# Kernel tuning notes

Measured on AMD Instinct MI355X. Metric: run time of the kernel, lower is better.

The kernel has to match this reference:

```python
import jax, jax.numpy as jnp
import numpy as np

EPS = 1e-12  # matches torch F.normalize default eps


def _l2_normalize(x, axis=-1):
    norm = jnp.sqrt(jnp.sum(x * x, axis=axis, keepdims=True))
    return x / jnp.maximum(norm, EPS)


def setup_inputs() -> dict:
    key = jax.random.key(0)
    k1, k2 = jax.random.split(key)
    B, D, P = 8192, 512, 32768
    z_context = jax.random.normal(k1, (B, D), dtype=jnp.float32)
    prototypes = jax.random.normal(k2, (P, D), dtype=jnp.float32) * 0.02
    return {"z_context": z_context, "prototypes": prototypes, "topk": 3}


def reference(z_context, prototypes, topk):
    # Cosine similarity: normalize queries and prototype bank, then GEMM.
    z_norm = _l2_normalize(z_context, axis=-1)          # [B, D]
    p_norm = _l2_normalize(prototypes, axis=-1)         # [P, D]
    sim = jnp.einsum('bd,pd->bp', z_norm, p_norm)       # [B, P]
    k = min(topk, prototypes.shape[0])
    topk_val, topk_idx = jax.lax.top_k(sim, k)          # [B, k] each
    return sim, topk_idx, topk_val
```

## Files before the change

kernel.cpp:

```cpp
#include <hip/hip_runtime.h>
#include <float.h>
#include <stdint.h>

#define D_DIM 512

typedef __attribute__((ext_vector_type(8))) short bf16x8;
typedef __attribute__((ext_vector_type(4))) float f32x4;

#define GLD_LDS16(g, l)                                              \
    __builtin_amdgcn_global_load_lds(                                \
        (const __attribute__((address_space(1))) void*)(g),          \
        (__attribute__((address_space(3))) void*)(l), 16, 0, 0)

__device__ __forceinline__ uint32_t pk_bf16(float a, float b) {
    uint32_t ua = __builtin_bit_cast(uint32_t, a) + 0x8000u;
    uint32_t ub = __builtin_bit_cast(uint32_t, b) + 0x8000u;
    return (ua >> 16) | (ub & 0xFFFF0000u);
}

#define INS4(val, idx, tv, ti)                                        \
    if ((val) > tv[3]) {                                              \
        int p_ = 3;                                                   \
        if ((val) > tv[2]) { tv[3] = tv[2]; ti[3] = ti[2]; p_ = 2; }  \
        if ((val) > tv[1]) { tv[2] = tv[1]; ti[2] = ti[1]; p_ = 1; }  \
        if ((val) > tv[0]) { tv[1] = tv[0]; ti[1] = ti[0]; p_ = 0; }  \
        tv[p_] = (val); ti[p_] = (idx);                               \
    }

__global__ __launch_bounds__(256) void convert_norm_kernel(
        const float* __restrict__ X, unsigned short* __restrict__ Xb,
        float* __restrict__ r, int R) {
    int row = blockIdx.x * 4 + (threadIdx.x >> 6);
    if (row >= R) return;
    int lane = threadIdx.x & 63;
    const float* x = X + (size_t)row * D_DIM + lane * 8;
    float4 f0 = *(const float4*)(x);
    float4 f1 = *(const float4*)(x + 4);
    float s = f0.x*f0.x + f0.y*f0.y + f0.z*f0.z + f0.w*f0.w
            + f1.x*f1.x + f1.y*f1.y + f1.z*f1.z + f1.w*f1.w;
#pragma unroll
    for (int off = 32; off; off >>= 1) s += __shfl_xor(s, off);
    float rv = 1.0f / fmaxf(sqrtf(s), 1e-12f);
    if (lane == 0) r[row] = rv;
    uint4 w;
    w.x = pk_bf16(f0.x * rv, f0.y * rv);
    w.y = pk_bf16(f0.z * rv, f0.w * rv);
    w.z = pk_bf16(f1.x * rv, f1.y * rv);
    w.w = pk_bf16(f1.z * rv, f1.w * rv);
    *(uint4*)(Xb + (size_t)row * D_DIM + lane * 8) = w;
}

__global__ __launch_bounds__(512, 2) void gemm256_fused(
        const unsigned short* __restrict__ Zb,
        const unsigned short* __restrict__ Pb,
        float* __restrict__ sim, uint2* __restrict__ part, int Pn) {
    extern __shared__ __align__(16) unsigned char SH[];
    uint4* S = (uint4*)SH;

    int bi = blockIdx.x;
    int mb, nb;
    if (gridDim.x == 4096) {
        int xcd = bi & 7, r = bi >> 3;
        mb = xcd * 4 + (r & 3);
        nb = r >> 2;
    } else {
        int nt = Pn >> 8;
        nb = bi % nt; mb = bi / nt;
    }
    const int bm = mb << 8, bn = nb << 8;

    const int tid = threadIdx.x;
    const int lane = tid & 63;
    const int wid = tid >> 6;
    const int wr = wid >> 2;
    const int wc = wid & 3;
    const int ln15 = lane & 15, hi = lane >> 4;

    const int fl0 = tid, fl1 = 512 + tid;
    const int rl0 = fl0 >> 3, rl1 = fl1 >> 3;
    const int cg0 = (fl0 & 7) ^ (rl0 & 7);
    const int cg1 = (fl1 & 7) ^ (rl1 & 7);

    const unsigned short* pA0q0 = Zb + (size_t)(bm + rl0) * D_DIM + cg0 * 8;
    const unsigned short* pA0q1 = Zb + (size_t)(bm + rl1) * D_DIM + cg1 * 8;
    const unsigned short* pA1q0 = Zb + (size_t)(bm + 128 + rl0) * D_DIM + cg0 * 8;
    const unsigned short* pA1q1 = Zb + (size_t)(bm + 128 + rl1) * D_DIM + cg1 * 8;
    const unsigned short* pB0q0 = Pb + (size_t)(bn + rl0) * D_DIM + cg0 * 8;
    const unsigned short* pB0q1 = Pb + (size_t)(bn + rl1) * D_DIM + cg1 * 8;
    const unsigned short* pB1q0 = Pb + (size_t)(bn + 128 + rl0) * D_DIM + cg0 * 8;
    const unsigned short* pB1q1 = Pb + (size_t)(bn + 128 + rl1) * D_DIM + cg1 * 8;

    const int dA0q0 = fl0,        dA0q1 = fl1;
    const int dA1q0 = 1024 + fl0, dA1q1 = 1024 + fl1;
    const int dB0q0 = 4096 + fl0, dB0q1 = 4096 + fl1;
    const int dB1q0 = 5120 + fl0, dB1q1 = 5120 + fl1;

    const int sw0 = hi ^ (ln15 & 7);
    const int sw1 = (4 + hi) ^ (ln15 & 7);
    int aOff[8], bOff[4];
#pragma unroll
    for (int m = 0; m < 8; ++m) aOff[m] = (wr * 128 + m * 16 + ln15) * 8;
#pragma unroll
    for (int n = 0; n < 4; ++n) bOff[n] = 4096 + (wc * 64 + n * 16 + ln15) * 8;

    f32x4 acc[8][4] = {};

    GLD_LDS16(pA0q0, &S[dA0q0]); GLD_LDS16(pA0q1, &S[dA0q1]);
    GLD_LDS16(pA1q0, &S[dA1q0]); GLD_LDS16(pA1q1, &S[dA1q1]);
    GLD_LDS16(pB0q0, &S[dB0q0]); GLD_LDS16(pB0q1, &S[dB0q1]);
    GLD_LDS16(pB1q0, &S[dB1q0]); GLD_LDS16(pB1q1, &S[dB1q1]);
    pA0q0 += 64; pA0q1 += 64; pA1q0 += 64; pA1q1 += 64;
    pB0q0 += 64; pB0q1 += 64; pB1q0 += 64; pB1q1 += 64;
    asm volatile("s_waitcnt vmcnt(0)" ::: "memory");
    __builtin_amdgcn_s_barrier();

#pragma unroll 1
    for (int t = 0; t < 8; ++t) {
        const int db = (t & 1) * 2048;
        const int dn = ((t + 1) & 1) * 2048;
        const bool more = (t < 7);
#pragma unroll
        for (int p = 0; p < 4; ++p) {
            const int mh = p >> 1, nh = p & 1;
            bf16x8 av[4][2], bv[2][2];
#pragma unroll
            for (int mi = 0; mi < 4; ++mi) {
                av[mi][0] = __builtin_bit_cast(bf16x8, S[db + aOff[mh * 4 + mi] + sw0]);
                av[mi][1] = __builtin_bit_cast(bf16x8, S[db + aOff[mh * 4 + mi] + sw1]);
            }
#pragma unroll
            for (int ni = 0; ni < 2; ++ni) {
                bv[ni][0] = __builtin_bit_cast(bf16x8, S[db + bOff[nh * 2 + ni] + sw0]);
                bv[ni][1] = __builtin_bit_cast(bf16x8, S[db + bOff[nh * 2 + ni] + sw1]);
            }
            if (p == 0 && more) {
                GLD_LDS16(pB0q0, &S[dn + dB0q0]); GLD_LDS16(pB0q1, &S[dn + dB0q1]);
                GLD_LDS16(pA0q0, &S[dn + dA0q0]); GLD_LDS16(pA0q1, &S[dn + dA0q1]);
                pB0q0 += 64; pB0q1 += 64; pA0q0 += 64; pA0q1 += 64;
            }
            if (p == 1 && more) {
                GLD_LDS16(pB1q0, &S[dn + dB1q0]); GLD_LDS16(pB1q1, &S[dn + dB1q1]);
                GLD_LDS16(pA1q0, &S[dn + dA1q0]); GLD_LDS16(pA1q1, &S[dn + dA1q1]);
                pB1q0 += 64; pB1q1 += 64; pA1q0 += 64; pA1q1 += 64;
            }
            __builtin_amdgcn_s_barrier();
            asm volatile("s_waitcnt lgkmcnt(0)" ::: "memory");
            __builtin_amdgcn_sched_barrier(0);
            __builtin_amdgcn_s_setprio(1);
#pragma unroll
            for (int kk = 0; kk < 2; ++kk)
#pragma unroll
                for (int mi = 0; mi < 4; ++mi)
#pragma unroll
                    for (int ni = 0; ni < 2; ++ni)
                        acc[mh * 4 + mi][nh * 2 + ni] =
                            __builtin_amdgcn_mfma_f32_16x16x32_bf16(
                                av[mi][kk], bv[ni][kk],
                                acc[mh * 4 + mi][nh * 2 + ni], 0, 0, 0);
            __builtin_amdgcn_s_setprio(0);
            __builtin_amdgcn_sched_barrier(0);
            if (p < 3) __builtin_amdgcn_s_barrier();
        }
        if (more) asm volatile("s_waitcnt vmcnt(0)" ::: "memory");
        __builtin_amdgcn_s_barrier();
    }

    float* T = (float*)SH;
    const int NB = Pn >> 8;
    const int r = tid >> 2;
    const int g = tid & 3;
#pragma unroll 1
    for (int hf = 0; hf < 2; ++hf) {
        float tv[4]; int ti[4];
#pragma unroll
        for (int k = 0; k < 4; ++k) { tv[k] = -FLT_MAX; ti[k] = 0x7FFFFFFF; }
#pragma unroll 1
        for (int ch = 0; ch < 2; ++ch) {
            __syncthreads();
            if (wr == hf && (wc >> 1) == ch) {
#pragma unroll
                for (int m = 0; m < 8; ++m)
#pragma unroll
                    for (int n = 0; n < 4; ++n)
                        *(f32x4*)&T[((wc & 1) * 64 + n * 16 + ln15) * 132
                                    + m * 16 + hi * 4] = acc[m][n];
            }
            __syncthreads();
            const int colBase = bn + ch * 128;
            float* srow = sim + (size_t)(bm + hf * 128 + r) * Pn + colBase;
#pragma unroll
            for (int j = 0; j < 8; ++j) {
                const int c0 = j * 16 + g * 4;
                float e0 = T[(c0 + 0) * 132 + r];
                float e1 = T[(c0 + 1) * 132 + r];
                float e2 = T[(c0 + 2) * 132 + r];
                float e3 = T[(c0 + 3) * 132 + r];
                float4 o; o.x = e0; o.y = e1; o.z = e2; o.w = e3;
                *(float4*)&srow[c0] = o;
                float mg = fmaxf(fmaxf(e0, e1), fmaxf(e2, e3));
                if (mg > tv[3]) {
                    INS4(e0, colBase + c0 + 0, tv, ti);
                    INS4(e1, colBase + c0 + 1, tv, ti);
                    INS4(e2, colBase + c0 + 2, tv, ti);
                    INS4(e3, colBase + c0 + 3, tv, ti);
                }
            }
        }
#pragma unroll
        for (int st = 1; st <= 2; st <<= 1) {
            float ov0 = __shfl_xor(tv[0], st), ov1 = __shfl_xor(tv[1], st);
            float ov2 = __shfl_xor(tv[2], st), ov3 = __shfl_xor(tv[3], st);
            int oi0 = __shfl_xor(ti[0], st), oi1 = __shfl_xor(ti[1], st);
            int oi2 = __shfl_xor(ti[2], st), oi3 = __shfl_xor(ti[3], st);
            INS4(ov0, oi0, tv, ti);
            INS4(ov1, oi1, tv, ti);
            INS4(ov2, oi2, tv, ti);
            INS4(ov3, oi3, tv, ti);
        }
        if (g == 0) {
            size_t o = ((size_t)(bm + hf * 128 + r) * NB + nb) * 4;
#pragma unroll
            for (int k = 0; k < 4; ++k)
                part[o + k] =
                    make_uint2(__builtin_bit_cast(uint32_t, tv[k]), (uint32_t)ti[k]);
        }
    }
}

__global__ __launch_bounds__(256) void topk_reduce(const uint2* __restrict__ part,
        const float* __restrict__ Z, const float* __restrict__ Pm,
        const float* __restrict__ rz, const float* __restrict__ rp,
        float* __restrict__ oidx, float* __restrict__ oval, int Pn, int NB) {
    int row = blockIdx.x * 4 + (threadIdx.x >> 6);
    int lane = threadIdx.x & 63;
    const uint2* pr = part + (size_t)row * NB * 4;

    float v[8]; int ix[8];
#pragma unroll
    for (int j = 0; j < 8; ++j) { v[j] = -FLT_MAX; ix[j] = -1; }

    const int total = NB * 4;
    for (int c = lane; c < total; c += 64) {
        uint2 u = pr[c];
        float val = __builtin_bit_cast(float, u.x);
        if (val > v[7]) {
            int idx = (int)u.y;
            int pos = 7;
#pragma unroll
            for (int j = 6; j >= 0; --j) {
                if (val > v[j]) { v[j+1] = v[j]; ix[j+1] = ix[j]; pos = j; }
            }
            v[pos] = val; ix[pos] = idx;
        }
    }

    int cand[8];
#pragma unroll
    for (int k = 0; k < 8; ++k) {
        float bv = v[0]; int bi2 = ix[0];
#pragma unroll
        for (int off = 32; off; off >>= 1) {
            float ov = __shfl_xor(bv, off);
            int oi = __shfl_xor(bi2, off);
            if (ov > bv || (ov == bv && oi >= 0 && (unsigned)oi < (unsigned)bi2)) {
                bv = ov; bi2 = oi;
            }
        }
        cand[k] = bi2;
        if (bi2 == ix[0]) {
#pragma unroll
            for (int j = 0; j < 7; ++j) { v[j] = v[j+1]; ix[j] = ix[j+1]; }
            v[7] = -FLT_MAX; ix[7] = -1;
        }
    }

    float zv[8];
    const float* zrow = Z + (size_t)row * D_DIM + lane * 8;
#pragma unroll
    for (int j = 0; j < 8; ++j) zv[j] = zrow[j];
    float rzv = rz[row];

    float ex[8];
#pragma unroll
    for (int c = 0; c < 8; ++c) {
        int idx = cand[c];
        const float* prow = Pm + (size_t)idx * D_DIM + lane * 8;
        float s = 0.f;
#pragma unroll
        for (int j = 0; j < 8; ++j) s += zv[j] * prow[j];
#pragma unroll
        for (int off = 32; off; off >>= 1) s += __shfl_xor(s, off);
        ex[c] = s * rzv * rp[idx];
    }

    bool used[8] = {};
#pragma unroll
    for (int k = 0; k < 3; ++k) {
        float bv = -FLT_MAX; int bi2 = Pn; int bc = 0;
#pragma unroll
        for (int c = 0; c < 8; ++c) {
            if (!used[c] && (ex[c] > bv || (ex[c] == bv && cand[c] < bi2))) {
                bv = ex[c]; bi2 = cand[c]; bc = c;
            }
        }
        used[bc] = true;
        if (lane == 0) {
            oidx[(size_t)row * 3 + k] = (float)bi2;
            oval[(size_t)row * 3 + k] = bv;
        }
    }
}

template <bool FUSE>
__global__ __launch_bounds__(256, 4) void gemm_lds_bf16(
        const unsigned short* __restrict__ Zb,
        const unsigned short* __restrict__ Pb,
        float* __restrict__ sim, uint2* __restrict__ part, int Pn) {
    __shared__ __align__(16) unsigned char SHs[32768];
    uint4* S = (uint4*)SHs;

    int bi = blockIdx.x;
    int mb, nb;
    if (gridDim.x == 16384) {
        int xcd = bi & 7;
        int r = bi >> 3;
        mb = xcd * 8 + (r & 7);
        nb = r >> 3;
    } else {
        nb = bi % (Pn / 128);
        mb = bi / (Pn / 128);
    }
    const int bm = mb * 128, bn = nb * 128;

    const int tid = threadIdx.x;
    const int lane = tid & 63;
    const int wid = tid >> 6;
    const int wr = wid >> 1, wc = wid & 1;
    const int ln15 = lane & 15, hi = lane >> 4;

    const unsigned short* gA[2];
    const unsigned short* gB[2];
    int ldsIdx[2];
#pragma unroll
    for (int q = 0; q < 2; ++q) {
        int flat = q * 256 + tid;
        int row = flat >> 2;
        int c = flat & 3;
        int cg = c ^ (row & 3);
        gA[q] = Zb + (size_t)(bm + row) * D_DIM + cg * 8;
        gB[q] = Pb + (size_t)(bn + row) * D_DIM + cg * 8;
        ldsIdx[q] = flat;
    }

    f32x4 acc[4][4] = {};

#pragma unroll
    for (int q = 0; q < 2; ++q) {
        GLD_LDS16(gA[q], &S[ldsIdx[q]]);
        GLD_LDS16(gB[q], &S[512 + ldsIdx[q]]);
        gA[q] += 32;
        gB[q] += 32;
    }

    int cur = 0;
#pragma unroll 1
    for (int s8 = 0; s8 < 16; ++s8) {
        const int nxt = cur ^ 1;
        if (s8 < 15) {
#pragma unroll
            for (int q = 0; q < 2; ++q) {
                GLD_LDS16(gA[q], &S[nxt * 1024 + ldsIdx[q]]);
                GLD_LDS16(gB[q], &S[nxt * 1024 + 512 + ldsIdx[q]]);
                gA[q] += 32;
                gB[q] += 32;
            }
            asm volatile("s_waitcnt vmcnt(4)" ::: "memory");
        } else {
            asm volatile("s_waitcnt vmcnt(0)" ::: "memory");
        }
        __builtin_amdgcn_s_barrier();
        __builtin_amdgcn_sched_barrier(0);

        const int sb = cur * 1024;
        __builtin_amdgcn_s_setprio(1);
        bf16x8 av[4], bv[4];
#pragma unroll
        for (int t = 0; t < 4; ++t) {
            int arow = wr * 64 + t * 16 + ln15;
            av[t] = __builtin_bit_cast(bf16x8,
                    S[sb + arow * 4 + (hi ^ (arow & 3))]);
            int brow = wc * 64 + t * 16 + ln15;
            bv[t] = __builtin_bit_cast(bf16x8,
                    S[sb + 512 + brow * 4 + (hi ^ (brow & 3))]);
        }
#pragma unroll
        for (int i = 0; i < 4; ++i)
#pragma unroll
            for (int j = 0; j < 4; ++j)
                acc[i][j] = __builtin_amdgcn_mfma_f32_16x16x32_bf16(
                    av[i], bv[j], acc[i][j], 0, 0, 0);
        __builtin_amdgcn_s_setprio(0);
        __builtin_amdgcn_sched_barrier(0);
        __builtin_amdgcn_s_barrier();
        cur = nxt;
    }

#pragma unroll
    for (int i = 0; i < 4; ++i) {
#pragma unroll
        for (int rr = 0; rr < 4; ++rr) {
            int row = bm + wr * 64 + i * 16 + hi * 4 + rr;
#pragma unroll
            for (int j = 0; j < 4; ++j) {
                int col = bn + wc * 64 + j * 16 + ln15;
                sim[(size_t)row * Pn + col] = acc[i][j][rr];
            }
        }
    }

    if constexpr (FUSE) {
        float* T = (float*)SHs;
        uint2* M = (uint2*)(SHs + 17408);
        const int NB = Pn >> 7;
        const int r = tid & 63;
        const int q = tid >> 6;
#pragma unroll 1
        for (int hf = 0; hf < 2; ++hf) {
            float rv[4]; int ri[4];
#pragma unroll
            for (int k = 0; k < 4; ++k) { rv[k] = -FLT_MAX; ri[k] = 0x7FFFFFFF; }
#pragma unroll 1
            for (int ch = 0; ch < 2; ++ch) {
                __syncthreads();
                if (wr == hf && wc == ch) {
#pragma unroll
                    for (int i = 0; i < 4; ++i)
#pragma unroll
                        for (int j = 0; j < 4; ++j)
                            *(f32x4*)&T[(j * 16 + ln15) * 68 + i * 16 + hi * 4]
                                = acc[i][j];
                }
                __syncthreads();
                float tv[4]; int ti[4];
#pragma unroll
                for (int k = 0; k < 4; ++k) { tv[k] = -FLT_MAX; ti[k] = 0x7FFFFFFF; }
#pragma unroll
                for (int c4 = 0; c4 < 16; c4 += 4) {
                    float e0 = T[(q * 16 + c4 + 0) * 68 + r];
                    float e1 = T[(q * 16 + c4 + 1) * 68 + r];
                    float e2 = T[(q * 16 + c4 + 2) * 68 + r];
                    float e3 = T[(q * 16 + c4 + 3) * 68 + r];
                    float mg = fmaxf(fmaxf(e0, e1), fmaxf(e2, e3));
                    if (mg > tv[3]) {
                        int cb = bn + ch * 64 + q * 16 + c4;
                        INS4(e0, cb + 0, tv, ti);
                        INS4(e1, cb + 1, tv, ti);
                        INS4(e2, cb + 2, tv, ti);
                        INS4(e3, cb + 3, tv, ti);
                    }
                }
#pragma unroll
                for (int k = 0; k < 4; ++k)
                    M[q * 256 + k * 64 + r] =
                        make_uint2(__builtin_bit_cast(uint32_t, tv[k]), (uint32_t)ti[k]);
                __syncthreads();
                if (tid < 64) {
#pragma unroll
                    for (int qq = 0; qq < 4; ++qq)
#pragma unroll
                        for (int k = 0; k < 4; ++k) {
                            uint2 u = M[qq * 256 + k * 64 + tid];
                            float val = __builtin_bit_cast(float, u.x);
                            INS4(val, (int)u.y, rv, ri);
                        }
                }
            }
            if (tid < 64) {
                size_t o = ((size_t)(bm + hf * 64 + tid) * NB + nb) * 4;
#pragma unroll
                for (int k = 0; k < 4; ++k)
                    part[o + k] =
                        make_uint2(__builtin_bit_cast(uint32_t, rv[k]), (uint32_t)ri[k]);
            }
        }
    }
}

__global__ __launch_bounds__(256) void rnorm_kernel(const float* __restrict__ X,
                                                    float* __restrict__ r, int R) {
    int row = blockIdx.x * 4 + (threadIdx.x >> 6);
    if (row >= R) return;
    int lane = threadIdx.x & 63;
    const float* x = X + (size_t)row * D_DIM;
    float s = 0.f;
#pragma unroll
    for (int t = 0; t < 2; ++t) {
        float4 v = *(const float4*)(x + (t * 64 + lane) * 4);
        s += v.x * v.x + v.y * v.y + v.z * v.z + v.w * v.w;
    }
#pragma unroll
    for (int off = 32; off; off >>= 1) s += __shfl_xor(s, off);
    if (lane == 0) r[row] = 1.0f / fmaxf(sqrtf(s), 1e-12f);
}

__global__ __launch_bounds__(256, 2) void gemm_bf16_sim(const float* __restrict__ Z,
        const float* __restrict__ Pm, const float* __restrict__ rz,
        const float* __restrict__ rp, float* __restrict__ sim, int Pn) {
    __shared__ uint4 As16[1024];
    __shared__ uint4 Bs16[1024];
    int bi = blockIdx.x;
    int nb = bi % (Pn / 128);
    int mb = bi / (Pn / 128);
    const int bm = mb * 128, bn = nb * 128;
    const int tid = threadIdx.x;
    const int srow = tid >> 1;
    const int half = tid & 1;
    const float* aP = Z  + (size_t)(bm + srow) * D_DIM + half * 32;
    const float* bP = Pm + (size_t)(bn + srow) * D_DIM + half * 32;
    const int lane = tid & 63;
    const int wid = tid >> 6;
    const int wr = wid >> 1, wc = wid & 1;
    const int ln15 = lane & 15, hi = lane >> 4;
    f32x4 acc[4][4] = {};
    float4 f[8], g[8];
#pragma unroll
    for (int q = 0; q < 8; ++q) {
        f[q] = *(const float4*)(aP + q * 4);
        g[q] = *(const float4*)(bP + q * 4);
    }
#pragma unroll 1
    for (int s = 0; s < 8; ++s) {
#pragma unroll
        for (int q8 = 0; q8 < 4; ++q8) {
            uint4 wa, wb;
            wa.x = pk_bf16(f[2*q8].x,   f[2*q8].y);
            wa.y = pk_bf16(f[2*q8].z,   f[2*q8].w);
            wa.z = pk_bf16(f[2*q8+1].x, f[2*q8+1].y);
            wa.w = pk_bf16(f[2*q8+1].z, f[2*q8+1].w);
            wb.x = pk_bf16(g[2*q8].x,   g[2*q8].y);
            wb.y = pk_bf16(g[2*q8].z,   g[2*q8].w);
            wb.z = pk_bf16(g[2*q8+1].x, g[2*q8+1].y);
            wb.w = pk_bf16(g[2*q8+1].z, g[2*q8+1].w);
            int colByte = half * 64 + q8 * 16;
            int idx = srow * 8 + ((colByte ^ ((srow & 7) << 4)) >> 4);
            As16[idx] = wa;
            Bs16[idx] = wb;
        }
        __syncthreads();
        if (s < 7) {
            int k0 = (s + 1) * 64;
#pragma unroll
            for (int q = 0; q < 8; ++q) {
                f[q] = *(const float4*)(aP + k0 + q * 4);
                g[q] = *(const float4*)(bP + k0 + q * 4);
            }
        }
#pragma unroll
        for (int kk = 0; kk < 2; ++kk) {
            bf16x8 av[4], bv[4];
            const int cb = kk * 64 + hi * 16;
#pragma unroll
            for (int t = 0; t < 4; ++t) {
                int arow = wr * 64 + t * 16 + ln15;
                av[t] = __builtin_bit_cast(bf16x8,
                        As16[arow * 8 + ((cb ^ ((arow & 7) << 4)) >> 4)]);
                int brow = wc * 64 + t * 16 + ln15;
                bv[t] = __builtin_bit_cast(bf16x8,
                        Bs16[brow * 8 + ((cb ^ ((brow & 7) << 4)) >> 4)]);
            }
#pragma unroll
            for (int i = 0; i < 4; ++i)
#pragma unroll
                for (int j = 0; j < 4; ++j)
                    acc[i][j] = __builtin_amdgcn_mfma_f32_16x16x32_bf16(
                        av[i], bv[j], acc[i][j], 0, 0, 0);
        }
        __syncthreads();
    }
    float rpv[4];
#pragma unroll
    for (int j = 0; j < 4; ++j) rpv[j] = rp[bn + wc * 64 + j * 16 + ln15];
#pragma unroll
    for (int i = 0; i < 4; ++i) {
#pragma unroll
        for (int rr = 0; rr < 4; ++rr) {
            int row = bm + wr * 64 + i * 16 + hi * 4 + rr;
            float rzv = rz[row];
#pragma unroll
            for (int j = 0; j < 4; ++j) {
                int col = bn + wc * 64 + j * 16 + ln15;
                sim[(size_t)row * Pn + col] = acc[i][j][rr] * rzv * rpv[j];
            }
        }
    }
}

__global__ __launch_bounds__(256) void topk_refine(const float* __restrict__ sim,
        const float* __restrict__ Z, const float* __restrict__ Pm,
        const float* __restrict__ rz, const float* __restrict__ rp,
        float* __restrict__ oidx, float* __restrict__ oval, int Pn) {
    int row = blockIdx.x * 4 + (threadIdx.x >> 6);
    int lane = threadIdx.x & 63;
    const float* rptr = sim + (size_t)row * Pn;

    float v[8]; int ix[8];
#pragma unroll
    for (int j = 0; j < 8; ++j) { v[j] = -FLT_MAX; ix[j] = -1; }

    const int iters = Pn >> 8;
    for (int t = 0; t < iters; ++t) {
        int base = t * 256 + lane * 4;
        float4 q = *(const float4*)(rptr + base);
        float vals[4] = {q.x, q.y, q.z, q.w};
#pragma unroll
        for (int e = 0; e < 4; ++e) {
            float val = vals[e];
            if (val > v[7]) {
                int idx = base + e;
                int pos = 7;
#pragma unroll
                for (int j = 6; j >= 0; --j) {
                    if (val > v[j]) { v[j+1] = v[j]; ix[j+1] = ix[j]; pos = j; }
                }
                v[pos] = val; ix[pos] = idx;
            }
        }
    }

    int cand[8];
#pragma unroll
    for (int k = 0; k < 8; ++k) {
        float bv = v[0]; int bi2 = ix[0];
#pragma unroll
        for (int off = 32; off; off >>= 1) {
            float ov = __shfl_xor(bv, off);
            int oi = __shfl_xor(bi2, off);
            if (ov > bv || (ov == bv && oi >= 0 && (unsigned)oi < (unsigned)bi2)) {
                bv = ov; bi2 = oi;
            }
        }
        cand[k] = bi2;
        if (bi2 == ix[0]) {
#pragma unroll
            for (int j = 0; j < 7; ++j) { v[j] = v[j+1]; ix[j] = ix[j+1]; }
            v[7] = -FLT_MAX; ix[7] = -1;
        }
    }

    float zv[8];
    const float* zrow = Z + (size_t)row * D_DIM + lane * 8;
#pragma unroll
    for (int j = 0; j < 8; ++j) zv[j] = zrow[j];
    float rzv = rz[row];

    float ex[8];
#pragma unroll
    for (int c = 0; c < 8; ++c) {
        int idx = cand[c];
        const float* prow = Pm + (size_t)idx * D_DIM + lane * 8;
        float s = 0.f;
#pragma unroll
        for (int j = 0; j < 8; ++j) s += zv[j] * prow[j];
#pragma unroll
        for (int off = 32; off; off >>= 1) s += __shfl_xor(s, off);
        ex[c] = s * rzv * rp[idx];
    }

    bool used[8] = {};
#pragma unroll
    for (int k = 0; k < 3; ++k) {
        float bv = -FLT_MAX; int bi2 = Pn; int bc = 0;
#pragma unroll
        for (int c = 0; c < 8; ++c) {
            if (!used[c] && (ex[c] > bv || (ex[c] == bv && cand[c] < bi2))) {
                bv = ex[c]; bi2 = cand[c]; bc = c;
            }
        }
        used[bc] = true;
        if (lane == 0) {
            oidx[(size_t)row * 3 + k] = (float)bi2;
            oval[(size_t)row * 3 + k] = bv;
        }
    }
}

extern "C" void kernel_launch(void* const* d_in, const int* in_sizes, int n_in,
                              void* d_out, int out_size, void* d_ws, size_t ws_size,
                              hipStream_t stream) {
    const float* Z  = (const float*)d_in[0];
    const float* Pm = (const float*)d_in[1];
    const int B  = in_sizes[0] / D_DIM;
    const int Pn = in_sizes[1] / D_DIM;

    float* sim  = (float*)d_out;
    float* oidx = sim + (size_t)B * Pn;
    float* oval = oidx + (size_t)B * 3;

    float* rz = (float*)d_ws;
    float* rp = rz + B;
    unsigned short* Zb = (unsigned short*)(rp + Pn);
    unsigned short* Pb = Zb + (size_t)B * D_DIM;
    uint2* part = (uint2*)(Pb + (size_t)Pn * D_DIM);

    const size_t need_bf16 = (size_t)(B + Pn) * 4 + (size_t)(B + Pn) * D_DIM * 2;
    const size_t need256 = need_bf16 + (size_t)B * (Pn >> 8) * 4 * sizeof(uint2);
    const size_t need128 = need_bf16 + (size_t)B * (Pn >> 7) * 4 * sizeof(uint2);

    bool big = false;
    if ((B & 255) == 0 && (Pn & 255) == 0 && ws_size >= need256) {
        big = (hipFuncSetAttribute((const void*)gemm256_fused,
                   hipFuncAttributeMaxDynamicSharedMemorySize,
                   131072) == hipSuccess);
    }

    if (big) {
        convert_norm_kernel<<<B / 4, 256, 0, stream>>>(Z, Zb, rz, B);
        convert_norm_kernel<<<Pn / 4, 256, 0, stream>>>(Pm, Pb, rp, Pn);
        gemm256_fused<<<(B / 256) * (Pn / 256), 512, 131072, stream>>>(
            Zb, Pb, sim, part, Pn);
        topk_reduce<<<B / 4, 256, 0, stream>>>(part, Z, Pm, rz, rp,
                                               oidx, oval, Pn, Pn >> 8);
    } else if (ws_size >= need128) {
        convert_norm_kernel<<<B / 4, 256, 0, stream>>>(Z, Zb, rz, B);
        convert_norm_kernel<<<Pn / 4, 256, 0, stream>>>(Pm, Pb, rp, Pn);
        gemm_lds_bf16<true><<<(B / 128) * (Pn / 128), 256, 0, stream>>>(
            Zb, Pb, sim, part, Pn);
        topk_reduce<<<B / 4, 256, 0, stream>>>(part, Z, Pm, rz, rp,
                                               oidx, oval, Pn, Pn >> 7);
    } else if (ws_size >= need_bf16) {
        convert_norm_kernel<<<B / 4, 256, 0, stream>>>(Z, Zb, rz, B);
        convert_norm_kernel<<<Pn / 4, 256, 0, stream>>>(Pm, Pb, rp, Pn);
        gemm_lds_bf16<false><<<(B / 128) * (Pn / 128), 256, 0, stream>>>(
            Zb, Pb, sim, nullptr, Pn);
        topk_refine<<<B / 4, 256, 0, stream>>>(sim, Z, Pm, rz, rp, oidx, oval, Pn);
    } else {
        rnorm_kernel<<<B / 4, 256, 0, stream>>>(Z, rz, B);
        rnorm_kernel<<<Pn / 4, 256, 0, stream>>>(Pm, rp, Pn);
        gemm_bf16_sim<<<(B / 128) * (Pn / 128), 256, 0, stream>>>(
            Z, Pm, rz, rp, sim, Pn);
        topk_refine<<<B / 4, 256, 0, stream>>>(sim, Z, Pm, rz, rp, oidx, oval, Pn);
    }
}
```

Before: 699.3 us.

## Use four-stage K=32 LDS pipeline and nontemporal stores for sim output

The main loop moves from a two-buffer K=64 pipeline to a four-buffer ring of K=32 stages. Three stages of global-to-LDS loads are kept in flight, with vmcnt waits matched to the number of outstanding loads. The per-stage sub-phase split and the extra barriers inside each stage are removed, and the swizzle changes to a 4-group XOR. The sim matrix writes now use nontemporal stores to avoid polluting the cache. Each stage does less MFMA work per barrier, so synchronisation overhead per unit of compute may go up.

```diff
diff --git a/kernel.cpp b/kernel.cpp
--- a/kernel.cpp
+++ b/kernel.cpp
@@ -76,94 +76,71 @@
     const int wc = wid & 3;
     const int ln15 = lane & 15, hi = lane >> 4;
 
-    const int fl0 = tid, fl1 = 512 + tid;
-    const int rl0 = fl0 >> 3, rl1 = fl1 >> 3;
-    const int cg0 = (fl0 & 7) ^ (rl0 & 7);
-    const int cg1 = (fl1 & 7) ^ (rl1 & 7);
-
-    const unsigned short* pA0q0 = Zb + (size_t)(bm + rl0) * D_DIM + cg0 * 8;
-    const unsigned short* pA0q1 = Zb + (size_t)(bm + rl1) * D_DIM + cg1 * 8;
-    const unsigned short* pA1q0 = Zb + (size_t)(bm + 128 + rl0) * D_DIM + cg0 * 8;
-    const unsigned short* pA1q1 = Zb + (size_t)(bm + 128 + rl1) * D_DIM + cg1 * 8;
-    const unsigned short* pB0q0 = Pb + (size_t)(bn + rl0) * D_DIM + cg0 * 8;
-    const unsigned short* pB0q1 = Pb + (size_t)(bn + rl1) * D_DIM + cg1 * 8;
-    const unsigned short* pB1q0 = Pb + (size_t)(bn + 128 + rl0) * D_DIM + cg0 * 8;
-    const unsigned short* pB1q1 = Pb + (size_t)(bn + 128 + rl1) * D_DIM + cg1 * 8;
-
-    const int dA0q0 = fl0,        dA0q1 = fl1;
-    const int dA1q0 = 1024 + fl0, dA1q1 = 1024 + fl1;
-    const int dB0q0 = 4096 + fl0, dB0q1 = 4096 + fl1;
-    const int dB1q0 = 5120 + fl0, dB1q1 = 5120 + fl1;
-
-    const int sw0 = hi ^ (ln15 & 7);
-    const int sw1 = (4 + hi) ^ (ln15 & 7);
+    const int f0 = tid, f1 = 512 + tid;
+    const int r0 = f0 >> 2, r1 = f1 >> 2;
+    const int cg0 = (f0 & 3) ^ (r0 & 3);
+    const int cg1 = (f1 & 3) ^ (r1 & 3);
+
+    const unsigned short* pA0 = Zb + (size_t)(bm + r0) * D_DIM + cg0 * 8;
+    const unsigned short* pA1 = Zb + (size_t)(bm + r1) * D_DIM + cg1 * 8;
+    const unsigned short* pB0 = Pb + (size_t)(bn + r0) * D_DIM + cg0 * 8;
+    const unsigned short* pB1 = Pb + (size_t)(bn + r1) * D_DIM + cg1 * 8;
+
+#define ISSUE(qb)                                                    \
+    do {                                                             \
+        GLD_LDS16(pA0, &S[(qb) * 2048 + f0]);                        \
+        GLD_LDS16(pA1, &S[(qb) * 2048 + f1]);                        \
+        GLD_LDS16(pB0, &S[(qb) * 2048 + 1024 + f0]);                 \
+        GLD_LDS16(pB1, &S[(qb) * 2048 + 1024 + f1]);                 \
+        pA0 += 32; pA1 += 32; pB0 += 32; pB1 += 32;                  \
+    } while (0)
+
+    const int sw = hi ^ (ln15 & 3);
     int aOff[8], bOff[4];
 #pragma unroll
-    for (int m = 0; m < 8; ++m) aOff[m] = (wr * 128 + m * 16 + ln15) * 8;
-#pragma unroll
-    for (int n = 0; n < 4; ++n) bOff[n] = 4096 + (wc * 64 + n * 16 + ln15) * 8;
+    for (int m = 0; m < 8; ++m) aOff[m] = (wr * 128 + m * 16 + ln15) * 4 + sw;
+#pragma unroll
+    for (int n = 0; n < 4; ++n) bOff[n] = 1024 + (wc * 64 + n * 16 + ln15) * 4 + sw;
 
     f32x4 acc[8][4] = {};
 
-    GLD_LDS16(pA0q0, &S[dA0q0]); GLD_LDS16(pA0q1, &S[dA0q1]);
-    GLD_LDS16(pA1q0, &S[dA1q0]); GLD_LDS16(pA1q1, &S[dA1q1]);
-    GLD_LDS16(pB0q0, &S[dB0q0]); GLD_LDS16(pB0q1, &S[dB0q1]);
-    GLD_LDS16(pB1q0, &S[dB1q0]); GLD_LDS16(pB1q1, &S[dB1q1]);
-    pA0q0 += 64; pA0q1 += 64; pA1q0 += 64; pA1q1 += 64;
-    pB0q0 += 64; pB0q1 += 64; pB1q0 += 64; pB1q1 += 64;
-    asm volatile("s_waitcnt vmcnt(0)" ::: "memory");
+    ISSUE(0); ISSUE(1); ISSUE(2);
+    asm volatile("s_waitcnt vmcnt(8)" ::: "memory");
     __builtin_amdgcn_s_barrier();
 
 #pragma unroll 1
-    for (int t = 0; t < 8; ++t) {
-        const int db = (t & 1) * 2048;
-        const int dn = ((t + 1) & 1) * 2048;
-        const bool more = (t < 7);
-#pragma unroll
-        for (int p = 0; p < 4; ++p) {
-            const int mh = p >> 1, nh = p & 1;
-            bf16x8 av[4][2], bv[2][2];
-#pragma unroll
-            for (int mi = 0; mi < 4; ++mi) {
-                av[mi][0] = __builtin_bit_cast(bf16x8, S[db + aOff[mh * 4 + mi] + sw0]);
-                av[mi][1] = __builtin_bit_cast(bf16x8, S[db + aOff[mh * 4 + mi] + sw1]);
-            }
-#pragma unroll
-            for (int ni = 0; ni < 2; ++ni) {
-                bv[ni][0] = __builtin_bit_cast(bf16x8, S[db + bOff[nh * 2 + ni] + sw0]);
-                bv[ni][1] = __builtin_bit_cast(bf16x8, S[db + bOff[nh * 2 + ni] + sw1]);
-            }
-            if (p == 0 && more) {
-                GLD_LDS16(pB0q0, &S[dn + dB0q0]); GLD_LDS16(pB0q1, &S[dn + dB0q1]);
-                GLD_LDS16(pA0q0, &S[dn + dA0q0]); GLD_LDS16(pA0q1, &S[dn + dA0q1]);
-                pB0q0 += 64; pB0q1 += 64; pA0q0 += 64; pA0q1 += 64;
-            }
-            if (p == 1 && more) {
-                GLD_LDS16(pB1q0, &S[dn + dB1q0]); GLD_LDS16(pB1q1, &S[dn + dB1q1]);
-                GLD_LDS16(pA1q0, &S[dn + dA1q0]); GLD_LDS16(pA1q1, &S[dn + dA1q1]);
-                pB1q0 += 64; pB1q1 += 64; pA1q0 += 64; pA1q1 += 64;
-            }
-            __builtin_amdgcn_s_barrier();
-            asm volatile("s_waitcnt lgkmcnt(0)" ::: "memory");
-            __builtin_amdgcn_sched_barrier(0);
-            __builtin_amdgcn_s_setprio(1);
-#pragma unroll
-            for (int kk = 0; kk < 2; ++kk)
-#pragma unroll
-                for (int mi = 0; mi < 4; ++mi)
-#pragma unroll
-                    for (int ni = 0; ni < 2; ++ni)
-                        acc[mh * 4 + mi][nh * 2 + ni] =
-                            __builtin_amdgcn_mfma_f32_16x16x32_bf16(
-                                av[mi][kk], bv[ni][kk],
-                                acc[mh * 4 + mi][nh * 2 + ni], 0, 0, 0);
-            __builtin_amdgcn_s_setprio(0);
-            __builtin_amdgcn_sched_barrier(0);
-            if (p < 3) __builtin_amdgcn_s_barrier();
-        }
-        if (more) asm volatile("s_waitcnt vmcnt(0)" ::: "memory");
+    for (int s = 0; s < 16; ++s) {
+        const int qb = s & 3;
+        bf16x8 av[8], bv[4];
+#pragma unroll
+        for (int mi = 0; mi < 8; ++mi)
+            av[mi] = __builtin_bit_cast(bf16x8, S[qb * 2048 + aOff[mi]]);
+#pragma unroll
+        for (int ni = 0; ni < 4; ++ni)
+            bv[ni] = __builtin_bit_cast(bf16x8, S[qb * 2048 + bOff[ni]]);
+        if (s < 13) {
+            ISSUE((s + 3) & 3);
+            asm volatile("s_waitcnt vmcnt(8)" ::: "memory");
+        } else if (s == 13) {
+            asm volatile("s_waitcnt vmcnt(4)" ::: "memory");
+        } else {
+            asm volatile("s_waitcnt vmcnt(0)" ::: "memory");
+        }
         __builtin_amdgcn_s_barrier();
-    }
+        asm volatile("s_waitcnt lgkmcnt(0)" ::: "memory");
+        __builtin_amdgcn_sched_barrier(0);
+        __builtin_amdgcn_s_setprio(1);
+#pragma unroll
+        for (int mi = 0; mi < 8; ++mi)
+#pragma unroll
+            for (int ni = 0; ni < 4; ++ni)
+                acc[mi][ni] = __builtin_amdgcn_mfma_f32_16x16x32_bf16(
+                    av[mi], bv[ni], acc[mi][ni], 0, 0, 0);
+        __builtin_amdgcn_s_setprio(0);
+        __builtin_amdgcn_sched_barrier(0);
+        __builtin_amdgcn_s_barrier();
+    }
+#undef ISSUE
 
     float* T = (float*)SH;
     const int NB = Pn >> 8;
@@ -195,8 +172,8 @@
                 float e1 = T[(c0 + 1) * 132 + r];
                 float e2 = T[(c0 + 2) * 132 + r];
                 float e3 = T[(c0 + 3) * 132 + r];
-                float4 o; o.x = e0; o.y = e1; o.z = e2; o.w = e3;
-                *(float4*)&srow[c0] = o;
+                f32x4 o; o[0] = e0; o[1] = e1; o[2] = e2; o[3] = e3;
+                __builtin_nontemporal_store(o, (f32x4*)&srow[c0]);
                 float mg = fmaxf(fmaxf(e0, e1), fmaxf(e2, e3));
                 if (mg > tv[3]) {
                     INS4(e0, colBase + c0 + 0, tv, ti);
```

New measurement: 682.6 us. 1.02x faster.
